# Kernel tuning notes

Measured on AMD Instinct MI355X. Metric: run time of the kernel, lower is better.

The kernel has to match this reference:

```python
import jax, jax.numpy as jnp
import numpy as np

B, T, Fd, C, D = 16, 256, 128, 32, 32
K_RATIO = 0.5
EPS = 1e-5


def setup_inputs() -> dict:
    key = jax.random.key(0)
    ks = jax.random.split(key, 40)
    n = lambda i, shape, s=0.05: jax.random.normal(ks[i], shape, jnp.float32) * s
    inp = {"x": jax.random.normal(ks[0], (B, T, Fd, C), jnp.float32)}
    inp.update(c1w=n(1, (C, C)), c1b=n(2, (C,)), bng=1.0 + n(3, (C,)), bnb=n(4, (C,)),
               bnm=n(5, (C,)), bnv=jax.random.uniform(ks[6], (C,)) + 0.5,
               c2w=n(7, (1, C)), c2b=n(8, (1,)))
    def gat_params(i0, pre):
        return {pre + "apw": n(i0, (D, C)), pre + "apb": n(i0 + 1, (D,)),
                pre + "aw": n(i0 + 2, (D,)), pre + "pww": n(i0 + 3, (D, C)),
                pre + "pwb": n(i0 + 4, (D,)), pre + "pow": n(i0 + 5, (D, C)),
                pre + "pob": n(i0 + 6, (D,)), pre + "g": 1.0 + n(i0 + 7, (D,)),
                pre + "be": n(i0 + 8, (D,)), pre + "m": n(i0 + 9, (D,)),
                pre + "v": jax.random.uniform(ks[i0 + 10], (D,)) + 0.5}
    inp.update(gat_params(9, "fc_"))
    inp.update(gat_params(20, "tc_"))
    inp.update(pfw=n(31, (1, D)), pfb=n(32, (1,)), ptw=n(33, (1, D)), ptb=n(34, (1,)),
               w1=n(35, (D, D)), w2=n(36, (D, D)), fcw=n(37, (2, 2 * D)), fcb=n(38, (2,)))
    return inp


def _gat(h, apw, apb, aw, pww, pwb, poww, pob, g, be, mu, var):
    # h: (B, N, C). Dense pairwise multiplication -> (B, N, N, C)
    p = h[:, :, None, :] * h[:, None, :, :]
    e = jnp.tanh(jnp.einsum('bijc,dc->bijd', p, apw) + apb)      # (B,N,N,D)
    att = jax.nn.softmax(jnp.einsum('bijd,d->bij', e, aw), axis=2)  # softmax over dim=-2 (temp=1)
    out = jnp.einsum('bij,bjc->bic', att, h) @ pww.T + pwb + h @ poww.T + pob
    out = (out - mu) / jnp.sqrt(var + EPS) * g + be               # BatchNorm1d (eval)
    return jax.nn.selu(out)


def _pool(h, pw, pb, ratio):
    s = jax.nn.sigmoid(h @ pw.T + pb)                # (B,N,1)
    kn = max(int(h.shape[1] * ratio), 1)
    _, idx = jax.lax.top_k(s[..., 0], kn)            # (B,kn), descending scores
    return jnp.take_along_axis(h * s, idx[..., None], axis=1)


def reference(x, c1w, c1b, bng, bnb, bnm, bnv, c2w, c2b,
              fc_apw, fc_apb, fc_aw, fc_pww, fc_pwb, fc_pow, fc_pob, fc_g, fc_be, fc_m, fc_v,
              tc_apw, tc_apb, tc_aw, tc_pww, tc_pwb, tc_pow, tc_pob, tc_g, tc_be, tc_m, tc_v,
              pfw, pfb, ptw, ptb, w1, w2, fcw, fcb):
    # conv1 (1x1), SELU, BatchNorm2d (eval), conv2 (1x1 -> 1 channel)
    xp = jnp.einsum('oc,btfc->botf', c1w, x) + c1b[None, :, None, None]
    xp = jax.nn.selu(xp)
    xp = (xp - bnm[None, :, None, None]) / jnp.sqrt(bnv + EPS)[None, :, None, None] \
         * bng[None, :, None, None] + bnb[None, :, None, None]
    m = jnp.einsum('c,bctf->btf', c2w[0], xp) + c2b[0]           # (B,T,F)
    M0 = jax.nn.softmax(m, axis=1)
    FCatt = jnp.einsum('btf,btfc->bfc', M0, x)                   # sum over T
    TCatt = jnp.einsum('btf,btfc->btc', M0, x)                   # sum over F
    FC_gat = _gat(FCatt, fc_apw, fc_apb, fc_aw, fc_pww, fc_pwb, fc_pow, fc_pob, fc_g, fc_be, fc_m, fc_v)
    TC_gat = _gat(TCatt, tc_apw, tc_apb, tc_aw, tc_pww, tc_pwb, tc_pow, tc_pob, tc_g, tc_be, tc_m, tc_v)
    xF = _pool(FC_gat, pfw, pfb, K_RATIO)                        # (B, F/2, D)
    xT = _pool(TC_gat, ptw, ptb, K_RATIO)                        # (B, T/2, D)
    M1 = jax.nn.softmax((xF @ w1.T) @ xT.transpose(0, 2, 1), axis=-1)
    M2 = jax.nn.softmax((xT @ w2.T) @ xF.transpose(0, 2, 1), axis=-1)
    xF_fused = xF + M1 @ xT
    xT_fused = xT + M2 @ xF
    node = jnp.concatenate([xF_fused.max(axis=1), xT_fused.max(axis=1)], axis=-1)
    return node @ fcw.T + fcb
```

## Files before the change

### kernel.cpp

```cpp
#include <hip/hip_runtime.h>
#include <hip/hip_bf16.h>

#define Bn 16
#define Tn 256
#define Fn 128
#define Cn 32
#define Dn 32
#define EPSf 1e-5f
#define SELU_L 1.0507009873554805f
#define SELU_A 1.6732632423543772f

typedef unsigned short u16;
typedef unsigned int u32;
typedef __attribute__((ext_vector_type(8))) short bf16x8;
typedef __attribute__((ext_vector_type(4))) float f32x4;

struct Ptrs { const void* p[39]; };

#define P_C1W 0
#define P_C1B 1024
#define P_MW  1056
#define P_MK  1088
#define P_FC  1089
#define P_TCG (1089+3264)
#define G_APW 0
#define G_APB 1024
#define G_AW  1056
#define G_PWW 1088
#define G_PWB 2112
#define G_POW 2144
#define G_POB 3168
#define G_GS  3200
#define G_GB  3232
#define GAT_SZ 3264
#define P_PFW (P_TCG+GAT_SZ)
#define P_PFB (P_PFW+32)
#define P_PTW (P_PFB+1)
#define P_PTB (P_PTW+32)
#define P_W1  (P_PTB+1)
#define P_W2  (P_W1+1024)
#define P_FCW (P_W2+1024)
#define P_FCB (P_FCW+128)
#define P_FLAG 10000

#define WS_M     10240
#define WS_FCATT (WS_M+524288)
#define WS_TCATT (WS_FCATT+65536)
#define WS_FCGAT (WS_TCATT+131072)
#define WS_TCGAT (WS_FCGAT+65536)
#define WS_XF    (WS_TCGAT+131072)
#define WS_XT    (WS_XF+32768)
#define WS_XFF   (WS_XT+65536)
#define WS_XTF   (WS_XFF+32768)

__device__ __forceinline__ float bf2f(u16 u) {
    union { u32 i; float f; } v; v.i = ((u32)u) << 16; return v.f;
}
__device__ __forceinline__ u16 f2bf(float f) {
    union { float f; u32 u; } v; v.f = f;
    u32 r = (v.u + 0x7fffu + ((v.u >> 16) & 1u)) >> 16;
    return (u16)r;
}
__device__ __forceinline__ void up2(u32 u, float* o) {
    union { u32 i; float f; } a, b;
    a.i = u << 16; b.i = u & 0xffff0000u;
    o[0] = a.f; o[1] = b.f;
}
__device__ __forceinline__ float tanh_fast(float x) {
    float e = __expf(2.f * x);
    return 1.f - 2.f / (e + 1.f);
}
__device__ __forceinline__ float ldp(const void* p, int i, int isb) {
    return isb ? bf2f(((const u16*)p)[i]) : ((const float*)p)[i];
}

__global__ __launch_bounds__(256) void k0_setup(Ptrs in, float* __restrict__ P) {
    __shared__ int sflag;
    int tid = threadIdx.x;
    int blk = blockIdx.x;
    if (tid < 64) {
        const u16* xu = (const u16*)in.p[0];
        int bad = 0;
        #pragma unroll
        for (int q = 0; q < 4; q++) {
            float f = bf2f(xu[tid * 4 + q]);
            float a = fabsf(f);
            if (!(a < 64.f) && !(a == 0.f)) bad++;
        }
        #pragma unroll
        for (int off = 32; off >= 1; off >>= 1) bad += __shfl_xor(bad, off, 64);
        if (tid == 0) sflag = (bad <= 8) ? 1 : 0;
    }
    __syncthreads();
    const int isb = sflag;

    if (blk == 0) {
        if (tid == 0) P[P_FLAG] = (float)isb;
        for (int i = tid; i < 1024; i += 256) P[P_C1W + i] = ldp(in.p[1], i, isb);
        if (tid < 32) {
            float A = ldp(in.p[3], tid, isb) * rsqrtf(ldp(in.p[6], tid, isb) + EPSf);
            float w = ldp(in.p[7], tid, isb);
            P[P_C1B + tid] = ldp(in.p[2], tid, isb);
            P[P_MW + tid] = w * A * SELU_L;
            float Bc = ldp(in.p[4], tid, isb) - ldp(in.p[5], tid, isb) * A;
            float term = w * Bc;
            #pragma unroll
            for (int off = 16; off >= 1; off >>= 1) term += __shfl_xor(term, off, 64);
            if (tid == 0) P[P_MK] = term + ldp(in.p[8], 0, isb);
        }
        if (tid >= 64 && tid < 96) {
            int t = tid - 64;
            P[P_PFW + t] = ldp(in.p[31], t, isb);
            P[P_PTW + t] = ldp(in.p[33], t, isb);
        }
        if (tid == 96) { P[P_PFB] = ldp(in.p[32], 0, isb); P[P_PTB] = ldp(in.p[34], 0, isb); }
        if (tid == 97) P[P_FCB]     = ldp(in.p[38], 0, isb);
        if (tid == 98) P[P_FCB + 1] = ldp(in.p[38], 1, isb);
        if (tid >= 128) P[P_FCW + (tid - 128)] = ldp(in.p[37], tid - 128, isb);
    } else if (blk <= 2) {
        int g = blk - 1;
        int ib = g ? 20 : 9;
        float* G = P + (g ? P_TCG : P_FC);
        for (int i = tid; i < 1024; i += 256) {
            G[G_APW + i] = ldp(in.p[ib + 0], i, isb);
            G[G_PWW + i] = ldp(in.p[ib + 3], i, isb);
            G[G_POW + i] = ldp(in.p[ib + 5], i, isb);
        }
        if (tid < 32) {
            G[G_APB + tid] = ldp(in.p[ib + 1], tid, isb);
            G[G_AW  + tid] = ldp(in.p[ib + 2], tid, isb);
            G[G_PWB + tid] = ldp(in.p[ib + 4], tid, isb);
            G[G_POB + tid] = ldp(in.p[ib + 6], tid, isb);
            float gs = ldp(in.p[ib + 7], tid, isb) * rsqrtf(ldp(in.p[ib + 10], tid, isb) + EPSf);
            G[G_GS + tid] = gs;
            G[G_GB + tid] = ldp(in.p[ib + 8], tid, isb) - ldp(in.p[ib + 9], tid, isb) * gs;
        }
    } else {
        for (int i = tid; i < 1024; i += 256) {
            P[P_W1 + i] = ldp(in.p[35], i, isb);
            P[P_W2 + i] = ldp(in.p[36], i, isb);
        }
    }
}

__global__ __launch_bounds__(256) void k1_conv_m(const void* __restrict__ xin,
                                                 const float* __restrict__ P,
                                                 float* __restrict__ M) {
    const int isb = __builtin_amdgcn_readfirstlane((int)P[P_FLAG]);
    int tid = threadIdx.x;
    if (isb) {
        int w = tid >> 6, lane = tid & 63;
        int n = lane & 15, g = lane >> 4, kc = g * 8;
        bf16x8 b0, b1;
        #pragma unroll
        for (int e = 0; e < 8; e++) {
            b0[e] = (short)f2bf(P[P_C1W + n * 32 + kc + e]);
            b1[e] = (short)f2bf(P[P_C1W + (n + 16) * 32 + kc + e]);
        }
        float cb0 = P[P_C1B + n], cb1 = P[P_C1B + n + 16];
        float mw0 = P[P_MW + n],  mw1 = P[P_MW + n + 16];
        float mk = P[P_MK];
        int rowblk = blockIdx.x * 256 + w * 64;
        const u16* xp = (const u16*)xin + (size_t)rowblk * 32;
        bf16x8 a[4];
        #pragma unroll
        for (int s = 0; s < 4; s++)
            a[s] = *(const bf16x8*)(xp + ((size_t)s * 16 + n) * 32 + kc);
        #pragma unroll
        for (int s = 0; s < 4; s++) {
            f32x4 c0 = {0.f, 0.f, 0.f, 0.f}, c1 = {0.f, 0.f, 0.f, 0.f};
            c0 = __builtin_amdgcn_mfma_f32_16x16x32_bf16(a[s], b0, c0, 0, 0, 0);
            c1 = __builtin_amdgcn_mfma_f32_16x16x32_bf16(a[s], b1, c1, 0, 0, 0);
            float acc[4];
            #pragma unroll
            for (int r = 0; r < 4; r++) {
                float z0 = c0[r] + cb0, z1 = c1[r] + cb1;
                float s0 = (z0 > 0.f) ? z0 : SELU_A * (__expf(z0) - 1.f);
                float s1 = (z1 > 0.f) ? z1 : SELU_A * (__expf(z1) - 1.f);
                acc[r] = fmaf(mw0, s0, mw1 * s1);
            }
            #pragma unroll
            for (int off = 1; off < 16; off <<= 1) {
                #pragma unroll
                for (int r = 0; r < 4; r++) acc[r] += __shfl_xor(acc[r], off, 64);
            }
            if (n == 0) {
                float4 o4 = make_float4(acc[0] + mk, acc[1] + mk, acc[2] + mk, acc[3] + mk);
                *(float4*)(M + (size_t)rowblk + s * 16 + g * 4) = o4;
            }
        }
    } else {
        int idx = blockIdx.x * 256 + tid;
        float xv[32];
        const float4* xf4 = reinterpret_cast<const float4*>((const float*)xin + (size_t)idx * 32);
        #pragma unroll
        for (int q = 0; q < 8; q++) {
            float4 v = xf4[q];
            xv[q * 4 + 0] = v.x; xv[q * 4 + 1] = v.y;
            xv[q * 4 + 2] = v.z; xv[q * 4 + 3] = v.w;
        }
        float acc = P[P_MK];
        #pragma unroll
        for (int o = 0; o < 32; o++) {
            float z = P[P_C1B + o];
            #pragma unroll
            for (int c = 0; c < 32; c++) z = fmaf(P[P_C1W + o * 32 + c], xv[c], z);
            float br = (z > 0.f) ? z : SELU_A * (__expf(z) - 1.f);
            acc = fmaf(P[P_MW + o], br, acc);
        }
        M[idx] = acc;
    }
}

__global__ __launch_bounds__(256) void k2_softmax(float* __restrict__ M,
                                                  float* __restrict__ FCzero) {
    __shared__ float r[256];
    int b = blockIdx.x >> 3, fg = blockIdx.x & 7;
    int tid = threadIdx.x;
    int fl = tid & 15, ts = tid >> 4;
    float* col = M + (size_t)b * (Tn * Fn) + fg * 16 + fl;
    float v[16];
    float mx = -1e30f;
    #pragma unroll
    for (int k = 0; k < 16; k++) { v[k] = col[(ts * 16 + k) * Fn]; mx = fmaxf(mx, v[k]); }
    r[tid] = mx; __syncthreads();
    for (int s = 128; s >= 16; s >>= 1) { if (tid < s) r[tid] = fmaxf(r[tid], r[tid + s]); __syncthreads(); }
    mx = r[fl];
    __syncthreads();
    float sm = 0.f;
    #pragma unroll
    for (int k = 0; k < 16; k++) { v[k] = __expf(v[k] - mx); sm += v[k]; }
    r[tid] = sm; __syncthreads();
    for (int s = 128; s >= 16; s >>= 1) { if (tid < s) r[tid] += r[tid + s]; __syncthreads(); }
    float inv = 1.f / r[fl];
    #pragma unroll
    for (int k = 0; k < 16; k++) col[(ts * 16 + k) * Fn] = v[k] * inv;
    int gid = blockIdx.x * 256 + tid;
    for (int i = gid; i < Bn * Fn * Cn; i += 128 * 256) FCzero[i] = 0.f;
}

__global__ __launch_bounds__(256) void k3n(const void* __restrict__ xin,
                                           const float* __restrict__ M,
                                           const float* __restrict__ Pflag,
                                           float* __restrict__ FCatt,
                                           float* __restrict__ TCatt) {
    __shared__ float part[4][8][32];
    int bi = blockIdx.x;
    int b = bi >> 5, tg = bi & 31;
    int tid = threadIdx.x;
    int w = tid >> 6, lane = tid & 63;
    const int isb = __builtin_amdgcn_readfirstlane((int)Pflag[P_FLAG]);
    float fa0[8], fa1[8];
    #pragma unroll
    for (int k = 0; k < 8; k++) { fa0[k] = 0.f; fa1[k] = 0.f; }
    int fbase = tid >> 4;
    for (int tt = 0; tt < 8; tt++) {
        int t = tg * 8 + tt;
        const float* Mrow = M + (size_t)b * (Tn * Fn) + (size_t)t * Fn;
        size_t rowoff = ((size_t)b * Tn + t) * (Fn * Cn);
        float ts0 = 0.f, ts1 = 0.f;
        #pragma unroll
        for (int k = 0; k < 8; k++) {
            float x0, x1;
            if (isb) {
                u32 u = *(const u32*)((const u16*)xin + rowoff + tid * 2 + 512 * k);
                float tmp[2]; up2(u, tmp); x0 = tmp[0]; x1 = tmp[1];
            } else {
                float2 v2 = *(const float2*)((const float*)xin + rowoff + tid * 2 + 512 * k);
                x0 = v2.x; x1 = v2.y;
            }
            float m = Mrow[fbase + 16 * k];
            x0 *= m; x1 *= m;
            fa0[k] += x0; fa1[k] += x1;
            ts0 += x0; ts1 += x1;
        }
        ts0 += __shfl_xor(ts0, 16, 64); ts0 += __shfl_xor(ts0, 32, 64);
        ts1 += __shfl_xor(ts1, 16, 64); ts1 += __shfl_xor(ts1, 32, 64);
        if (lane < 16) {
            part[w][tt][lane * 2]     = ts0;
            part[w][tt][lane * 2 + 1] = ts1;
        }
    }
    __syncthreads();
    {
        int tt = tid >> 5, c = tid & 31;
        float s = part[0][tt][c] + part[1][tt][c] + part[2][tt][c] + part[3][tt][c];
        TCatt[((size_t)b * Tn + tg * 8 + tt) * Cn + c] = s;
    }
    #pragma unroll
    for (int k = 0; k < 8; k++) {
        atomicAdd(&FCatt[(size_t)b * 4096 + tid * 2 + 512 * k],     fa0[k]);
        atomicAdd(&FCatt[(size_t)b * 4096 + tid * 2 + 512 * k + 1], fa1[k]);
    }
}

__global__ __launch_bounds__(256) void k4a_scores(const float* __restrict__ P,
                                                  const float* __restrict__ FCatt,
                                                  const float* __restrict__ TCatt,
                                                  u16* __restrict__ SFC,
                                                  u16* __restrict__ STC) {
    int bi = blockIdx.x;
    int tid = threadIdx.x;
    int w = tid >> 6, lane = tid & 63;
    int n = lane & 15, g = lane >> 4, kc = g * 8;
    int N, nt, b, i; const float* h; u16* S; const float* G;
    if (bi < 512) { N = 128; nt = 8; b = bi >> 5; i = (bi & 31) * 4 + w;
        h = FCatt + (size_t)b * 4096; S = SFC + (size_t)b * 16384; G = P + P_FC; }
    else { int t = bi - 512; N = 256; nt = 16; b = t >> 6; i = (t & 63) * 4 + w;
        h = TCatt + (size_t)b * 8192; S = STC + (size_t)b * 65536; G = P + P_TCG; }

    bf16x8 b0, b1;
    #pragma unroll
    for (int e = 0; e < 8; e++) {
        b0[e] = (short)f2bf(G[G_APW + n * 32 + kc + e]);
        b1[e] = (short)f2bf(G[G_APW + (n + 16) * 32 + kc + e]);
    }
    float aw0 = G[G_AW + n],  aw1 = G[G_AW + n + 16];
    float ab0 = G[G_APB + n], ab1 = G[G_APB + n + 16];

    float hi[8];
    {
        const float4* hip = (const float4*)(h + (size_t)i * 32 + kc);
        float4 v0 = hip[0], v1 = hip[1];
        hi[0] = v0.x; hi[1] = v0.y; hi[2] = v0.z; hi[3] = v0.w;
        hi[4] = v1.x; hi[5] = v1.y; hi[6] = v1.z; hi[7] = v1.w;
    }

    for (int jt = 0; jt < nt; jt++) {
        const float4* hjp = (const float4*)(h + ((size_t)jt * 16 + n) * 32 + kc);
        float4 v0 = hjp[0], v1 = hjp[1];
        float hj[8];
        hj[0] = v0.x; hj[1] = v0.y; hj[2] = v0.z; hj[3] = v0.w;
        hj[4] = v1.x; hj[5] = v1.y; hj[6] = v1.z; hj[7] = v1.w;
        bf16x8 a;
        #pragma unroll
        for (int e = 0; e < 8; e++) a[e] = (short)f2bf(hi[e] * hj[e]);
        f32x4 c0 = {0.f, 0.f, 0.f, 0.f}, c1 = {0.f, 0.f, 0.f, 0.f};
        c0 = __builtin_amdgcn_mfma_f32_16x16x32_bf16(a, b0, c0, 0, 0, 0);
        c1 = __builtin_amdgcn_mfma_f32_16x16x32_bf16(a, b1, c1, 0, 0, 0);
        float sc[4];
        #pragma unroll
        for (int r = 0; r < 4; r++)
            sc[r] = fmaf(aw0, tanh_fast(c0[r] + ab0), aw1 * tanh_fast(c1[r] + ab1));
        #pragma unroll
        for (int off = 1; off < 16; off <<= 1) {
            #pragma unroll
            for (int r = 0; r < 4; r++) sc[r] += __shfl_xor(sc[r], off, 64);
        }
        if (n == 0) {
            union { u16 q[4]; uint2 v; } pk;
            #pragma unroll
            for (int r = 0; r < 4; r++) pk.q[r] = f2bf(sc[r]);
            *(uint2*)(S + (size_t)i * N + jt * 16 + g * 4) = pk.v;
        }
    }
}

__global__ __launch_bounds__(256) void k4b_soft(const float* __restrict__ P,
                                                const float* __restrict__ FCatt,
                                                const float* __restrict__ TCatt,
                                                const u16* __restrict__ SFC,
                                                const u16* __restrict__ STC,
                                                float* __restrict__ FCgat,
                                                float* __restrict__ TCgat) {
    __shared__ float hs[256 * 32];
    __shared__ float scb[4][256];
    int bi = blockIdx.x;
    int N, b, rowbase; const float* h; float* out; const float* G; const u16* S;
    if (bi < 128) {
        N = 128; b = bi >> 3; rowbase = (bi & 7) * 16;
        h = FCatt + (size_t)b * 4096; out = FCgat + (size_t)b * 4096; G = P + P_FC;
        S = SFC + (size_t)b * 16384;
    } else {
        int t = bi - 128;
        N = 256; b = t >> 4; rowbase = (t & 15) * 16;
        h = TCatt + (size_t)b * 8192; out = TCgat + (size_t)b * 8192; G = P + P_TCG;
        S = STC + (size_t)b * 65536;
    }
    int tid = threadIdx.x;
    int w = tid >> 6, lane = tid & 63;
    const float4* h4 = reinterpret_cast<const float4*>(h);
    float4* hs4 = reinterpret_cast<float4*>(hs);
    for (int el = tid; el < N * 8; el += 256) hs4[el] = h4[el];
    __syncthreads();

    int c = lane & 31;
    int nq = N >> 6;
    for (int r = 0; r < 4; r++) {
        int row = rowbase + w + 4 * r;
        const u16* Srow = S + (size_t)row * N;
        float v[4];
        float mx = -1e30f;
        for (int q = 0; q < nq; q++) { v[q] = bf2f(Srow[lane + 64 * q]); mx = fmaxf(mx, v[q]); }
        #pragma unroll
        for (int off = 32; off >= 1; off >>= 1) mx = fmaxf(mx, __shfl_xor(mx, off, 64));
        float sum = 0.f;
        for (int q = 0; q < nq; q++) {
            float e = __expf(v[q] - mx);
            scb[w][lane + 64 * q] = e;
            sum += e;
        }
        #pragma unroll
        for (int off = 32; off >= 1; off >>= 1) sum += __shfl_xor(sum, off, 64);
        float inv = 1.f / sum;
        asm volatile("s_waitcnt lgkmcnt(0)" ::: "memory");
        int half = lane >> 5;
        float acc = 0.f;
        for (int j = half; j < N; j += 2) acc = fmaf(scb[w][j], hs[j * 32 + c], acc);
        acc += __shfl_xor(acc, 32, 64);
        acc *= inv;
        int d = c;
        float z = G[G_PWB + d] + G[G_POB + d];
        #pragma unroll
        for (int c2 = 0; c2 < 32; c2++)
            z = fmaf(G[G_PWW + d * 32 + c2], __shfl(acc, c2, 64),
                fmaf(G[G_POW + d * 32 + c2], hs[row * 32 + c2], z));
        z = z * G[G_GS + d] + G[G_GB + d];
        z = SELU_L * ((z > 0.f) ? z : SELU_A * (__expf(z) - 1.f));
        if (lane < 32) out[(size_t)row * 32 + d] = z;
    }
}

__global__ __launch_bounds__(256) void k5_pool(const float* __restrict__ P,
                                               const float* __restrict__ FCgat,
                                               const float* __restrict__ TCgat,
                                               float* __restrict__ XF,
                                               float* __restrict__ XT) {
    __shared__ float s[256];
    int bi = blockIdx.x;
    int N, kn, b, pboff; const float* g; float* xp; const float* pw;
    if (bi < 16) { b = bi; N = 128; kn = 64;
        g = FCgat + (size_t)b * 4096; xp = XF + (size_t)b * 2048; pw = P + P_PFW; pboff = P_PFB; }
    else { b = bi - 16; N = 256; kn = 128;
        g = TCgat + (size_t)b * 8192; xp = XT + (size_t)b * 4096; pw = P + P_PTW; pboff = P_PTB; }
    int tid = threadIdx.x;
    float sv = 0.f;
    if (tid < N) {
        float z = P[pboff];
        #pragma unroll
        for (int d = 0; d < 32; d++) z = fmaf(pw[d], g[(size_t)tid * 32 + d], z);
        sv = 1.f / (1.f + __expf(-z));
        s[tid] = sv;
    }
    __syncthreads();
    if (tid < N) {
        int rank = 0;
        for (int l = 0; l < N; l++) {
            float sl = s[l];
            rank += (sl > sv) || (sl == sv && l < tid);
        }
        if (rank < kn) {
            #pragma unroll
            for (int d = 0; d < 32; d++) xp[(size_t)rank * 32 + d] = g[(size_t)tid * 32 + d] * sv;
        }
    }
}

__global__ __launch_bounds__(256) void k6_fuse(const float* __restrict__ P,
                                               const float* __restrict__ XF,
                                               const float* __restrict__ XT,
                                               float* __restrict__ XFF,
                                               float* __restrict__ XTF) {
    int wid = blockIdx.x * 4 + (threadIdx.x >> 6);
    int lane = threadIdx.x & 63;
    if (wid < 1024) {
        int b = wid >> 6, i = wid & 63;
        const float* xf  = XF + ((size_t)b * 64 + i) * 32;
        const float* xtb = XT + (size_t)b * 4096;
        const float* w1 = P + P_W1;
        int d = lane & 31;
        float y = 0.f;
        #pragma unroll
        for (int c = 0; c < 32; c++) y = fmaf(w1[d * 32 + c], xf[c], y);
        float xtr0[32], xtr1[32];
        #pragma unroll
        for (int c = 0; c < 32; c++) {
            xtr0[c] = xtb[(size_t)lane * 32 + c];
            xtr1[c] = xtb[(size_t)(lane + 64) * 32 + c];
        }
        float s0 = 0.f, s1 = 0.f;
        #pragma unroll
        for (int c = 0; c < 32; c++) {
            float yc = __shfl(y, c, 64);
            s0 = fmaf(yc, xtr0[c], s0);
            s1 = fmaf(yc, xtr1[c], s1);
        }
        float mx = fmaxf(s0, s1);
        #pragma unroll
        for (int off = 1; off < 64; off <<= 1) mx = fmaxf(mx, __shfl_xor(mx, off, 64));
        float e0 = __expf(s0 - mx), e1 = __expf(s1 - mx);
        float sm = e0 + e1;
        #pragma unroll
        for (int off = 1; off < 64; off <<= 1) sm += __shfl_xor(sm, off, 64);
        float inv = 1.f / sm;
        float a0 = e0 * inv, a1 = e1 * inv;
        float v[32];
        #pragma unroll
        for (int c = 0; c < 32; c++) v[c] = a0 * xtr0[c] + a1 * xtr1[c];
        #pragma unroll
        for (int off = 1; off < 64; off <<= 1) {
            #pragma unroll
            for (int c = 0; c < 32; c++) v[c] += __shfl_xor(v[c], off, 64);
        }
        if (lane == 0) {
            float* o = XFF + ((size_t)b * 64 + i) * 32;
            #pragma unroll
            for (int c = 0; c < 32; c++) o[c] = xf[c] + v[c];
        }
    } else {
        int r = wid - 1024;
        int b = r >> 7, i = r & 127;
        const float* xt  = XT + ((size_t)b * 128 + i) * 32;
        const float* xfb = XF + (size_t)b * 2048;
        const float* w2 = P + P_W2;
        int d = lane & 31;
        float y = 0.f;
        #pragma unroll
        for (int c = 0; c < 32; c++) y = fmaf(w2[d * 32 + c], xt[c], y);
        float xfr[32];
        #pragma unroll
        for (int c = 0; c < 32; c++) xfr[c] = xfb[(size_t)lane * 32 + c];
        float sc0 = 0.f;
        #pragma unroll
        for (int c = 0; c < 32; c++) sc0 = fmaf(__shfl(y, c, 64), xfr[c], sc0);
        float mx = sc0;
        #pragma unroll
        for (int off = 1; off < 64; off <<= 1) mx = fmaxf(mx, __shfl_xor(mx, off, 64));
        float e = __expf(sc0 - mx);
        float sm = e;
        #pragma unroll
        for (int off = 1; off < 64; off <<= 1) sm += __shfl_xor(sm, off, 64);
        float a = e / sm;
        float v[32];
        #pragma unroll
        for (int c = 0; c < 32; c++) v[c] = a * xfr[c];
        #pragma unroll
        for (int off = 1; off < 64; off <<= 1) {
            #pragma unroll
            for (int c = 0; c < 32; c++) v[c] += __shfl_xor(v[c], off, 64);
        }
        if (lane == 0) {
            float* o = XTF + ((size_t)b * 128 + i) * 32;
            #pragma unroll
            for (int c = 0; c < 32; c++) o[c] = xt[c] + v[c];
        }
    }
}

__global__ __launch_bounds__(64) void k7_out(const float* __restrict__ P,
                                             const float* __restrict__ XFF,
                                             const float* __restrict__ XTF,
                                             void* __restrict__ outp) {
    __shared__ float node[64];
    int b = blockIdx.x, tid = threadIdx.x;
    if (tid < 32) {
        float m = -1e30f;
        for (int r = 0; r < 64; r++) m = fmaxf(m, XFF[((size_t)b * 64 + r) * 32 + tid]);
        node[tid] = m;
    } else {
        int c = tid - 32;
        float m = -1e30f;
        for (int r = 0; r < 128; r++) m = fmaxf(m, XTF[((size_t)b * 128 + r) * 32 + c]);
        node[tid] = m;
    }
    __syncthreads();
    if (tid < 2) {
        float z = P[P_FCB + tid];
        #pragma unroll
        for (int k = 0; k < 64; k++) z = fmaf(P[P_FCW + tid * 64 + k], node[k], z);
        int isb = (int)P[P_FLAG];
        if (isb) ((u16*)outp)[b * 2 + tid] = f2bf(z);
        else     ((float*)outp)[b * 2 + tid] = z;
    }
}

extern "C" void kernel_launch(void* const* d_in, const int* in_sizes, int n_in,
                              void* d_out, int out_size, void* d_ws, size_t ws_size,
                              hipStream_t stream) {
    (void)in_sizes; (void)n_in; (void)out_size; (void)ws_size;
    float* W = (float*)d_ws;
    Ptrs ptrs;
    for (int i = 0; i < 39; i++) ptrs.p[i] = d_in[i];
    const void* x = d_in[0];
    float* P = W;
    u16* STC = (u16*)(W + WS_M);
    u16* SFC = (u16*)(W + WS_XF);

    k0_setup<<<4, 256, 0, stream>>>(ptrs, P);
    k1_conv_m<<<2048, 256, 0, stream>>>(x, P, W + WS_M);
    k2_softmax<<<128, 256, 0, stream>>>(W + WS_M, W + WS_FCATT);
    k3n<<<512, 256, 0, stream>>>(x, W + WS_M, P, W + WS_FCATT, W + WS_TCATT);
    k4a_scores<<<1536, 256, 0, stream>>>(P, W + WS_FCATT, W + WS_TCATT, SFC, STC);
    k4b_soft<<<384, 256, 0, stream>>>(P, W + WS_FCATT, W + WS_TCATT, SFC, STC,
                                      W + WS_FCGAT, W + WS_TCGAT);
    k5_pool<<<32, 256, 0, stream>>>(P, W + WS_FCGAT, W + WS_TCGAT, W + WS_XF, W + WS_XT);
    k6_fuse<<<768, 256, 0, stream>>>(P, W + WS_XF, W + WS_XT, W + WS_XFF, W + WS_XTF);
    k7_out<<<16, 64, 0, stream>>>(P, W + WS_XFF, W + WS_XTF, d_out);
}
```

Baseline: 334.7 us.

## Transpose MFMA operands to cut shuffle reductions and split TC score rows

The MFMA operands in the conv and attention-score kernels are swapped so that output channels land along the register axis. This lets each lane reduce its 4 accumulator rows locally, so the 4-step 16-lane butterfly becomes a 2-step cross-group shuffle. bf16 conversion now uses the packed v_cvt_pk_bf16_f32 instruction. The TC score work is also split into half-rows (8 column tiles per wave), raising the k4a grid from 1536 to 2560 blocks for more parallelism, at the cost of redundant weight setup per wave and narrower 2-byte stores.

```diff
diff --git a/kernel.cpp b/kernel.cpp
--- a/kernel.cpp
+++ b/kernel.cpp
@@ -61,6 +61,11 @@
     u32 r = (v.u + 0x7fffu + ((v.u >> 16) & 1u)) >> 16;
     return (u16)r;
 }
+__device__ __forceinline__ u32 cvt_pk_bf16(float lo, float hi) {
+    u32 r;
+    asm("v_cvt_pk_bf16_f32 %0, %1, %2" : "=v"(r) : "v"(lo), "v"(hi));
+    return r;
+}
 __device__ __forceinline__ void up2(u32 u, float* o) {
     union { u32 i; float f; } a, b;
     a.i = u << 16; b.i = u & 0xffff0000u;
@@ -151,14 +156,22 @@
     if (isb) {
         int w = tid >> 6, lane = tid & 63;
         int n = lane & 15, g = lane >> 4, kc = g * 8;
-        bf16x8 b0, b1;
-        #pragma unroll
-        for (int e = 0; e < 8; e++) {
-            b0[e] = (short)f2bf(P[P_C1W + n * 32 + kc + e]);
-            b1[e] = (short)f2bf(P[P_C1W + (n + 16) * 32 + kc + e]);
-        }
-        float cb0 = P[P_C1B + n], cb1 = P[P_C1B + n + 16];
-        float mw0 = P[P_MW + n],  mw1 = P[P_MW + n + 16];
+        union { u32 u[4]; bf16x8 v; } B0, B1;
+        #pragma unroll
+        for (int e = 0; e < 4; e++) {
+            B0.u[e] = cvt_pk_bf16(P[P_C1W + n * 32 + kc + 2 * e],
+                                  P[P_C1W + n * 32 + kc + 2 * e + 1]);
+            B1.u[e] = cvt_pk_bf16(P[P_C1W + (n + 16) * 32 + kc + 2 * e],
+                                  P[P_C1W + (n + 16) * 32 + kc + 2 * e + 1]);
+        }
+        float cb0v[4], cb1v[4], mw0v[4], mw1v[4];
+        #pragma unroll
+        for (int r = 0; r < 4; r++) {
+            cb0v[r] = P[P_C1B + g * 4 + r];
+            cb1v[r] = P[P_C1B + 16 + g * 4 + r];
+            mw0v[r] = P[P_MW + g * 4 + r];
+            mw1v[r] = P[P_MW + 16 + g * 4 + r];
+        }
         float mk = P[P_MK];
         int rowblk = blockIdx.x * 256 + w * 64;
         const u16* xp = (const u16*)xin + (size_t)rowblk * 32;
@@ -169,25 +182,20 @@
         #pragma unroll
         for (int s = 0; s < 4; s++) {
             f32x4 c0 = {0.f, 0.f, 0.f, 0.f}, c1 = {0.f, 0.f, 0.f, 0.f};
-            c0 = __builtin_amdgcn_mfma_f32_16x16x32_bf16(a[s], b0, c0, 0, 0, 0);
-            c1 = __builtin_amdgcn_mfma_f32_16x16x32_bf16(a[s], b1, c1, 0, 0, 0);
-            float acc[4];
+            c0 = __builtin_amdgcn_mfma_f32_16x16x32_bf16(B0.v, a[s], c0, 0, 0, 0);
+            c1 = __builtin_amdgcn_mfma_f32_16x16x32_bf16(B1.v, a[s], c1, 0, 0, 0);
+            float part = 0.f;
             #pragma unroll
             for (int r = 0; r < 4; r++) {
-                float z0 = c0[r] + cb0, z1 = c1[r] + cb1;
+                float z0 = c0[r] + cb0v[r], z1 = c1[r] + cb1v[r];
                 float s0 = (z0 > 0.f) ? z0 : SELU_A * (__expf(z0) - 1.f);
                 float s1 = (z1 > 0.f) ? z1 : SELU_A * (__expf(z1) - 1.f);
-                acc[r] = fmaf(mw0, s0, mw1 * s1);
+                part = fmaf(mw0v[r], s0, part);
+                part = fmaf(mw1v[r], s1, part);
             }
-            #pragma unroll
-            for (int off = 1; off < 16; off <<= 1) {
-                #pragma unroll
-                for (int r = 0; r < 4; r++) acc[r] += __shfl_xor(acc[r], off, 64);
-            }
-            if (n == 0) {
-                float4 o4 = make_float4(acc[0] + mk, acc[1] + mk, acc[2] + mk, acc[3] + mk);
-                *(float4*)(M + (size_t)rowblk + s * 16 + g * 4) = o4;
-            }
+            part += __shfl_xor(part, 16, 64);
+            part += __shfl_xor(part, 32, 64);
+            if (lane < 16) M[(size_t)rowblk + s * 16 + n] = part + mk;
         }
     } else {
         int idx = blockIdx.x * 256 + tid;
@@ -303,20 +311,34 @@
     int tid = threadIdx.x;
     int w = tid >> 6, lane = tid & 63;
     int n = lane & 15, g = lane >> 4, kc = g * 8;
-    int N, nt, b, i; const float* h; u16* S; const float* G;
-    if (bi < 512) { N = 128; nt = 8; b = bi >> 5; i = (bi & 31) * 4 + w;
-        h = FCatt + (size_t)b * 4096; S = SFC + (size_t)b * 16384; G = P + P_FC; }
-    else { int t = bi - 512; N = 256; nt = 16; b = t >> 6; i = (t & 63) * 4 + w;
-        h = TCatt + (size_t)b * 8192; S = STC + (size_t)b * 65536; G = P + P_TCG; }
-
-    bf16x8 b0, b1;
+    int N, b, i, jt0; const float* h; u16* S; const float* G;
+    if (bi < 512) {
+        N = 128; b = bi >> 5; i = (bi & 31) * 4 + w; jt0 = 0;
+        h = FCatt + (size_t)b * 4096; S = SFC + (size_t)b * 16384; G = P + P_FC;
+    } else {
+        int unit = (bi - 512) * 4 + w;
+        N = 256; b = unit >> 9;
+        int rem = unit & 511;
+        i = rem >> 1; jt0 = (rem & 1) * 8;
+        h = TCatt + (size_t)b * 8192; S = STC + (size_t)b * 65536; G = P + P_TCG;
+    }
+
+    union { u32 u[4]; bf16x8 v; } B0, B1;
     #pragma unroll
-    for (int e = 0; e < 8; e++) {
-        b0[e] = (short)f2bf(G[G_APW + n * 32 + kc + e]);
-        b1[e] = (short)f2bf(G[G_APW + (n + 16) * 32 + kc + e]);
-    }
-    float aw0 = G[G_AW + n],  aw1 = G[G_AW + n + 16];
-    float ab0 = G[G_APB + n], ab1 = G[G_APB + n + 16];
+    for (int e = 0; e < 4; e++) {
+        B0.u[e] = cvt_pk_bf16(G[G_APW + n * 32 + kc + 2 * e],
+                              G[G_APW + n * 32 + kc + 2 * e + 1]);
+        B1.u[e] = cvt_pk_bf16(G[G_APW + (n + 16) * 32 + kc + 2 * e],
+                              G[G_APW + (n + 16) * 32 + kc + 2 * e + 1]);
+    }
+    float awv0[4], awv1[4], abv0[4], abv1[4];
+    #pragma unroll
+    for (int r = 0; r < 4; r++) {
+        awv0[r] = G[G_AW + g * 4 + r];
+        awv1[r] = G[G_AW + 16 + g * 4 + r];
+        abv0[r] = G[G_APB + g * 4 + r];
+        abv1[r] = G[G_APB + 16 + g * 4 + r];
+    }
 
     float hi[8];
     {
@@ -326,33 +348,28 @@
         hi[4] = v1.x; hi[5] = v1.y; hi[6] = v1.z; hi[7] = v1.w;
     }
 
-    for (int jt = 0; jt < nt; jt++) {
+    #pragma unroll 2
+    for (int q = 0; q < 8; q++) {
+        int jt = jt0 + q;
         const float4* hjp = (const float4*)(h + ((size_t)jt * 16 + n) * 32 + kc);
         float4 v0 = hjp[0], v1 = hjp[1];
-        float hj[8];
-        hj[0] = v0.x; hj[1] = v0.y; hj[2] = v0.z; hj[3] = v0.w;
-        hj[4] = v1.x; hj[5] = v1.y; hj[6] = v1.z; hj[7] = v1.w;
-        bf16x8 a;
-        #pragma unroll
-        for (int e = 0; e < 8; e++) a[e] = (short)f2bf(hi[e] * hj[e]);
+        union { u32 u[4]; bf16x8 v; } A;
+        A.u[0] = cvt_pk_bf16(hi[0] * v0.x, hi[1] * v0.y);
+        A.u[1] = cvt_pk_bf16(hi[2] * v0.z, hi[3] * v0.w);
+        A.u[2] = cvt_pk_bf16(hi[4] * v1.x, hi[5] * v1.y);
+        A.u[3] = cvt_pk_bf16(hi[6] * v1.z, hi[7] * v1.w);
         f32x4 c0 = {0.f, 0.f, 0.f, 0.f}, c1 = {0.f, 0.f, 0.f, 0.f};
-        c0 = __builtin_amdgcn_mfma_f32_16x16x32_bf16(a, b0, c0, 0, 0, 0);
-        c1 = __builtin_amdgcn_mfma_f32_16x16x32_bf16(a, b1, c1, 0, 0, 0);
-        float sc[4];
-        #pragma unroll
-        for (int r = 0; r < 4; r++)
-            sc[r] = fmaf(aw0, tanh_fast(c0[r] + ab0), aw1 * tanh_fast(c1[r] + ab1));
-        #pragma unroll
-        for (int off = 1; off < 16; off <<= 1) {
-            #pragma unroll
-            for (int r = 0; r < 4; r++) sc[r] += __shfl_xor(sc[r], off, 64);
-        }
-        if (n == 0) {
-            union { u16 q[4]; uint2 v; } pk;
-            #pragma unroll
-            for (int r = 0; r < 4; r++) pk.q[r] = f2bf(sc[r]);
-            *(uint2*)(S + (size_t)i * N + jt * 16 + g * 4) = pk.v;
-        }
+        c0 = __builtin_amdgcn_mfma_f32_16x16x32_bf16(B0.v, A.v, c0, 0, 0, 0);
+        c1 = __builtin_amdgcn_mfma_f32_16x16x32_bf16(B1.v, A.v, c1, 0, 0, 0);
+        float part = 0.f;
+        #pragma unroll
+        for (int r = 0; r < 4; r++) {
+            part = fmaf(awv0[r], tanh_fast(c0[r] + abv0[r]), part);
+            part = fmaf(awv1[r], tanh_fast(c1[r] + abv1[r]), part);
+        }
+        part += __shfl_xor(part, 16, 64);
+        part += __shfl_xor(part, 32, 64);
+        if (lane < 16) S[(size_t)i * N + jt * 16 + n] = f2bf(part);
     }
 }
 
@@ -590,7 +607,7 @@
     k1_conv_m<<<2048, 256, 0, stream>>>(x, P, W + WS_M);
     k2_softmax<<<128, 256, 0, stream>>>(W + WS_M, W + WS_FCATT);
     k3n<<<512, 256, 0, stream>>>(x, W + WS_M, P, W + WS_FCATT, W + WS_TCATT);
-    k4a_scores<<<1536, 256, 0, stream>>>(P, W + WS_FCATT, W + WS_TCATT, SFC, STC);
+    k4a_scores<<<2560, 256, 0, stream>>>(P, W + WS_FCATT, W + WS_TCATT, SFC, STC);
     k4b_soft<<<384, 256, 0, stream>>>(P, W + WS_FCATT, W + WS_TCATT, SFC, STC,
                                       W + WS_FCGAT, W + WS_TCGAT);
     k5_pool<<<32, 256, 0, stream>>>(P, W + WS_FCGAT, W + WS_TCGAT, W + WS_XF, W + WS_XT);
```

Measured after the change: 336.1 us. About the same (+0.4%).
